# Kernel optimization log

Measured on AMD Instinct MI355X. Metric: run time of the kernel, lower is better.

## Reference

```python
import jax, jax.numpy as jnp
import numpy as np

B, IN, H = 4096, 2048, 2048
STD = 1.0 / np.sqrt(H)


def setup_inputs() -> dict:
    key = jax.random.key(0)
    ks = jax.random.split(key, 16)
    uni = lambda k, shape: jax.random.uniform(k, shape, jnp.float32, -STD, STD)
    inp = {
        "x": jax.random.normal(ks[0], (B, IN), jnp.float32),
        "h": jax.random.normal(ks[1], (B, H), jnp.float32),
        "c": jax.random.normal(ks[2], (B, H), jnp.float32),
        # weights are used untransposed via th.mm(x, w): w_x* must be [IN, H]-compatible,
        # which in the original requires IN == H; shapes kept as [H, IN].
        "w_xi": uni(ks[3], (H, IN)), "w_xf": uni(ks[4], (H, IN)),
        "w_xo": uni(ks[5], (H, IN)), "w_xc": uni(ks[6], (H, IN)),
        "w_hi": uni(ks[7], (H, H)), "w_hf": uni(ks[8], (H, H)),
        "w_ho": uni(ks[9], (H, H)), "w_hc": uni(ks[10], (H, H)),
        "b_i": uni(ks[11], (H,)), "b_f": uni(ks[12], (H,)),
        "b_o": uni(ks[13], (H,)), "b_c": uni(ks[14], (H,)),
    }
    return inp


def reference(x, h, c, w_xi, w_xf, w_xo, w_xc, w_hi, w_hf, w_ho, w_hc,
              b_i, b_f, b_o, b_c):
    # Fused form of the 8 small GEMMs: concat gate weights along output dim.
    Wx = jnp.concatenate([w_xi, w_xf, w_xo, w_xc], axis=1)  # [IN, 4H]
    Wh = jnp.concatenate([w_hi, w_hf, w_ho, w_hc], axis=1)  # [H, 4H]
    b = jnp.concatenate([b_i, b_f, b_o, b_c])               # [4H]
    gates = x @ Wx + h @ Wh + b                              # [B, 4H]
    i_t, f_t, o_t, g_t = jnp.split(gates, 4, axis=1)
    i_t = jax.nn.sigmoid(i_t)
    f_t = jax.nn.sigmoid(f_t)
    o_t = jax.nn.sigmoid(o_t)
    g_t = jnp.tanh(g_t)
    c_t = c * f_t + i_t * g_t
    h_t = o_t * jnp.tanh(c_t)
    # original reshapes to [B, 1, H]
    return h_t[:, None, :], c_t[:, None, :]
```

## Files before the change

### kernel.cpp

```cpp
#include <hip/hip_runtime.h>
#include <stdint.h>

typedef unsigned short u16;
typedef __bf16 bf16x8 __attribute__((ext_vector_type(8)));
typedef float f32x4 __attribute__((ext_vector_type(4)));
typedef unsigned short u16x8 __attribute__((ext_vector_type(8)));
typedef unsigned short u16x4 __attribute__((ext_vector_type(4)));

#define B_ROWS 4096
#define H_DIM  2048
#define K_DIM  4096
#define N_DIM  8192

__device__ __forceinline__ u16 f2b(float f) {
  union { float f; unsigned int i; } v; v.f = f;
  unsigned int i = v.i;
  return (u16)((i + 0x7fffu + ((i >> 16) & 1u)) >> 16);
}
__device__ __forceinline__ float b2f(u16 u) {
  union { unsigned int i; float f; } v; v.i = ((unsigned int)u) << 16; return v.f;
}
__device__ __forceinline__ float sigmoidf_(float x) { return 1.0f / (1.0f + __expf(-x)); }
__device__ __forceinline__ float tanhf_(float x)    { return 1.0f - 2.0f / (__expf(2.0f * x) + 1.0f); }

__device__ __forceinline__ void glds16(const u16* g, u16* l) {
  __builtin_amdgcn_global_load_lds(
      (__attribute__((address_space(1))) void*)(g),
      (__attribute__((address_space(3))) void*)(l), 16, 0, 0);
}

__device__ __forceinline__ uint32_t lds_off(const void* p) {
  return (uint32_t)(uintptr_t)(__attribute__((address_space(3))) const void*)p;
}

__device__ __forceinline__ bf16x8 ds_read128(uint32_t byte_off) {
  bf16x8 r;
  asm volatile("ds_read_b128 %0, %1" : "=&v"(r) : "v"(byte_off));
  return r;
}
#define LGKM0   asm volatile("s_waitcnt lgkmcnt(0)" ::: "memory")
#define SCHED_FENCE __builtin_amdgcn_sched_barrier(0)

struct WPtrs { const float* p[8]; };

__global__ __launch_bounds__(256) void prep_all(WPtrs wp,
                                                const float* __restrict__ X,
                                                const float* __restrict__ Hs,
                                                u16* __restrict__ Wt,
                                                u16* __restrict__ Abf) {
  __shared__ float tile[64][65];
  const int z = blockIdx.z;
  const int tid = threadIdx.x;
  if (z < 8) {
    const int s = z >> 2, g = z & 3;
    const float* __restrict__ w = wp.p[z];
    const int j0 = blockIdx.x * 64, k0 = blockIdx.y * 64;

    const int c4 = (tid & 15) * 4;
    const int r0 = tid >> 4;
#pragma unroll
    for (int it = 0; it < 4; ++it) {
      int r = r0 + it * 16;
      float4 v = *(const float4*)(w + (size_t)(k0 + r) * H_DIM + j0 + c4);
      tile[r][c4 + 0] = v.x;
      tile[r][c4 + 1] = v.y;
      tile[r][c4 + 2] = v.z;
      tile[r][c4 + 3] = v.w;
    }
    __syncthreads();

    const int cc = (tid & 7) * 8;
    const int jr0 = tid >> 3;
#pragma unroll
    for (int it = 0; it < 2; ++it) {
      int jr = jr0 + it * 32;
      u16x8 v;
#pragma unroll
      for (int i = 0; i < 8; ++i) v[i] = f2b(tile[cc + i][jr]);
      size_t orow = (size_t)(g * H_DIM + j0 + jr);
      *(u16x8*)(Wt + orow * K_DIM + (size_t)(s * H_DIM + k0 + cc)) = v;
    }
  } else {
    const int cid = (z - 8) * 1024 + blockIdx.y * 32 + blockIdx.x;
#pragma unroll
    for (int t = 0; t < 4; ++t) {
      const size_t chunk = (size_t)cid * 1024 + t * 256 + tid;
      const int b = (int)(chunk >> 9);
      const int c = ((int)chunk & 511) * 8;
      const float* src = (c < H_DIM) ? (X + (size_t)b * H_DIM + c)
                                     : (Hs + (size_t)b * H_DIM + (c - H_DIM));
      float4 v0 = *(const float4*)(src);
      float4 v1 = *(const float4*)(src + 4);
      u16x8 o;
      o[0] = f2b(v0.x); o[1] = f2b(v0.y); o[2] = f2b(v0.z); o[3] = f2b(v0.w);
      o[4] = f2b(v1.x); o[5] = f2b(v1.y); o[6] = f2b(v1.z); o[7] = f2b(v1.w);
      *(u16x8*)(Abf + chunk * 8) = o;
    }
  }
}

__global__ __launch_bounds__(512, 2) void gemm_gates(const u16* __restrict__ A,
                                                     const u16* __restrict__ Wt,
                                                     u16* __restrict__ gates) {
  __shared__ __align__(16) u16 sA[4 * 256 * 32];
  __shared__ __align__(16) u16 sB[4 * 256 * 32];
  const int tid = threadIdx.x;
  const int wave = tid >> 6, lane = tid & 63;
  const int wm = wave >> 2, wn = wave & 3;

  const int wg = (blockIdx.x & 7) * 64 + (blockIdx.x >> 3);
  const int bm = wg & 15;
  const int bn = wg >> 4;

  const int c0 = wave * 2;
  const int rs0 = c0 * 16 + (lane >> 2);
  const int rs1 = rs0 + 16;
  const int kc0 = (lane & 3) ^ ((rs0 >> 1) & 3);
  const int kc1 = (lane & 3) ^ ((rs1 >> 1) & 3);
  const size_t gA0 = (size_t)(bm * 256 + rs0) * K_DIM + kc0 * 8;
  const size_t gA1 = (size_t)(bm * 256 + rs1) * K_DIM + kc1 * 8;
  const size_t gB0 = (size_t)(bn * 256 + rs0) * K_DIM + kc0 * 8;
  const size_t gB1 = (size_t)(bn * 256 + rs1) * K_DIM + kc1 * 8;

  const int q = lane >> 4;
  uint32_t aOffB[8], bOffB[4];
#pragma unroll
  for (int i = 0; i < 8; ++i) {
    int ra = wm * 128 + i * 16 + (lane & 15);
    aOffB[i] = (uint32_t)(ra * 32 + ((q ^ ((ra >> 1) & 3)) * 8)) * 2u;
  }
#pragma unroll
  for (int i = 0; i < 4; ++i) {
    int rb = wn * 64 + i * 16 + (lane & 15);
    bOffB[i] = (uint32_t)(rb * 32 + ((q ^ ((rb >> 1) & 3)) * 8)) * 2u;
  }
  const uint32_t sAb = lds_off(sA);
  const uint32_t sBb = lds_off(sB);

  f32x4 acc[8][4] = {};
  const int NT = K_DIM / 32;

#pragma unroll
  for (int t = 0; t < 3; ++t) {
    const size_t ko = (size_t)t * 32;
    u16* da = sA + t * 8192;
    u16* db = sB + t * 8192;
    glds16(A  + gA0 + ko, da + c0 * 512);
    glds16(A  + gA1 + ko, da + (c0 + 1) * 512);
    glds16(Wt + gB0 + ko, db + c0 * 512);
    glds16(Wt + gB1 + ko, db + (c0 + 1) * 512);
  }
  asm volatile("s_waitcnt vmcnt(8)" ::: "memory");
  __builtin_amdgcn_s_barrier();

  for (int T = 0; T < NT; ++T) {
    const uint32_t aSlot = sAb + (uint32_t)(T & 3) * 16384u;
    const uint32_t bSlot = sBb + (uint32_t)(T & 3) * 16384u;
    const int pf = T + 3;
    const bool dopf = pf < NT;
    const size_t ko = (size_t)pf * 32;
    u16* dA = sA + (pf & 3) * 8192;
    u16* dB = sB + (pf & 3) * 8192;

    if (dopf) {
      glds16(A + gA0 + ko, dA + c0 * 512);
      glds16(A + gA1 + ko, dA + (c0 + 1) * 512);
    }
    bf16x8 af[4], bf[4];
#pragma unroll
    for (int i = 0; i < 4; ++i) af[i] = ds_read128(aSlot + aOffB[i]);
#pragma unroll
    for (int i = 0; i < 4; ++i) bf[i] = ds_read128(bSlot + bOffB[i]);
    __builtin_amdgcn_s_barrier();
    LGKM0;
    SCHED_FENCE;
    __builtin_amdgcn_s_setprio(1);
#pragma unroll
    for (int mi = 0; mi < 4; ++mi)
#pragma unroll
      for (int ni = 0; ni < 4; ++ni)
        acc[mi][ni] = __builtin_amdgcn_mfma_f32_16x16x32_bf16(af[mi], bf[ni], acc[mi][ni], 0, 0, 0);
    __builtin_amdgcn_s_setprio(0);

    if (dopf) {
      glds16(Wt + gB0 + ko, dB + c0 * 512);
      glds16(Wt + gB1 + ko, dB + (c0 + 1) * 512);
    }
    bf16x8 ag[4];
#pragma unroll
    for (int i = 0; i < 4; ++i) ag[i] = ds_read128(aSlot + aOffB[4 + i]);
    __builtin_amdgcn_s_barrier();
    LGKM0;
    SCHED_FENCE;
    __builtin_amdgcn_s_setprio(1);
#pragma unroll
    for (int mi = 0; mi < 4; ++mi)
#pragma unroll
      for (int ni = 0; ni < 4; ++ni)
        acc[4 + mi][ni] = __builtin_amdgcn_mfma_f32_16x16x32_bf16(ag[mi], bf[ni], acc[4 + mi][ni], 0, 0, 0);
    __builtin_amdgcn_s_setprio(0);

    if (T < NT - 3)       { asm volatile("s_waitcnt vmcnt(8)" ::: "memory"); }
    else if (T == NT - 3) { asm volatile("s_waitcnt vmcnt(4)" ::: "memory"); }
    else if (T == NT - 2) { asm volatile("s_waitcnt vmcnt(0)" ::: "memory"); }
    if (T < NT - 1) __builtin_amdgcn_s_barrier();
  }

  const int rbase = bm * 256 + wm * 128 + (lane >> 4) * 4;
  const int cbase = bn * 256 + wn * 64 + (lane & 15);
#pragma unroll
  for (int mi = 0; mi < 8; ++mi) {
#pragma unroll
    for (int ni = 0; ni < 4; ++ni) {
      size_t base = (size_t)(rbase + mi * 16) * N_DIM + (size_t)(cbase + ni * 16);
#pragma unroll
      for (int r = 0; r < 4; ++r)
        gates[base + (size_t)r * N_DIM] = f2b(acc[mi][ni][r]);
    }
  }
}

__global__ __launch_bounds__(256) void lstm_epilogue(
    const u16* __restrict__ gates, const float* __restrict__ Cin,
    const float* __restrict__ Bi, const float* __restrict__ Bf,
    const float* __restrict__ Bo, const float* __restrict__ Bc,
    float* __restrict__ Out) {
  const int idx = blockIdx.x * 256 + threadIdx.x;
  const int b = idx >> 9;
  const int j = (idx & 511) * 4;
  const size_t gbase = (size_t)b * N_DIM + j;
  u16x4 iv = *(const u16x4*)(gates + gbase);
  u16x4 fv = *(const u16x4*)(gates + gbase + 2048);
  u16x4 ov = *(const u16x4*)(gates + gbase + 4096);
  u16x4 gv = *(const u16x4*)(gates + gbase + 6144);
  float4 cv  = *(const float4*)(Cin + (size_t)b * H_DIM + j);
  float4 biv = *(const float4*)(Bi + j);
  float4 bfv = *(const float4*)(Bf + j);
  float4 bov = *(const float4*)(Bo + j);
  float4 bcv = *(const float4*)(Bc + j);
  float ce[4] = {cv.x, cv.y, cv.z, cv.w};
  float bie[4] = {biv.x, biv.y, biv.z, biv.w};
  float bfe[4] = {bfv.x, bfv.y, bfv.z, bfv.w};
  float boe[4] = {bov.x, bov.y, bov.z, bov.w};
  float bce[4] = {bcv.x, bcv.y, bcv.z, bcv.w};
  float4 hv, ctv;
  float he[4], cte[4];
#pragma unroll
  for (int e = 0; e < 4; ++e) {
    float it = sigmoidf_(b2f(iv[e]) + bie[e]);
    float ft = sigmoidf_(b2f(fv[e]) + bfe[e]);
    float ot = sigmoidf_(b2f(ov[e]) + boe[e]);
    float gt = tanhf_(b2f(gv[e]) + bce[e]);
    float ct = ce[e] * ft + it * gt;
    he[e] = ot * tanhf_(ct);
    cte[e] = ct;
  }
  hv.x = he[0]; hv.y = he[1]; hv.z = he[2]; hv.w = he[3];
  ctv.x = cte[0]; ctv.y = cte[1]; ctv.z = cte[2]; ctv.w = cte[3];
  *(float4*)(Out + (size_t)b * H_DIM + j) = hv;
  *(float4*)(Out + (size_t)B_ROWS * H_DIM + (size_t)b * H_DIM + j) = ctv;
}

extern "C" void kernel_launch(void* const* d_in, const int* in_sizes, int n_in,
                              void* d_out, int out_size, void* d_ws, size_t ws_size,
                              hipStream_t stream) {
  const float* X   = (const float*)d_in[0];
  const float* Hs  = (const float*)d_in[1];
  const float* Cin = (const float*)d_in[2];
  WPtrs wp;
  for (int i = 0; i < 8; ++i) wp.p[i] = (const float*)d_in[3 + i];
  const float* Bi = (const float*)d_in[11];
  const float* Bf = (const float*)d_in[12];
  const float* Bo = (const float*)d_in[13];
  const float* Bc = (const float*)d_in[14];

  u16* Wt    = (u16*)d_ws;
  u16* Abf   = Wt + (size_t)N_DIM * K_DIM;
  u16* gates = Abf + (size_t)B_ROWS * K_DIM;
  float* Out = (float*)d_out;

  prep_all<<<dim3(32, 32, 10), 256, 0, stream>>>(wp, X, Hs, Wt, Abf);
  gemm_gates<<<16 * 32, 512, 0, stream>>>(Abf, Wt, gates);
  lstm_epilogue<<<(B_ROWS * H_DIM / 4) / 256, 256, 0, stream>>>(gates, Cin, Bi, Bf, Bo, Bc, Out);
}
```

Baseline: 519.2 us.

## Software-pipeline LDS fragment reads across K-tiles with double-buffered B registers

Restructures the GEMM main loop so the next tile's A and B fragments are read from LDS while the second half of the current tile's MFMAs runs. B fragments ping-pong between two register sets, which needs a two-tile unrolled loop. The upper A fragments use an immediate-offset ds_read instead of separate offset registers. One barrier per tile is removed, which reduces LDS-latency stalls and synchronization, at the cost of more live registers and a more fragile waitcnt and barrier schedule.

After: 506.7 us. 2.4% less time.

```diff
diff --git a/kernel.cpp b/kernel.cpp
--- a/kernel.cpp
+++ b/kernel.cpp
@@ -38,7 +38,11 @@
   asm volatile("ds_read_b128 %0, %1" : "=&v"(r) : "v"(byte_off));
   return r;
 }
-#define LGKM0   asm volatile("s_waitcnt lgkmcnt(0)" ::: "memory")
+__device__ __forceinline__ bf16x8 ds_read128_hi(uint32_t byte_off) {
+  bf16x8 r;
+  asm volatile("ds_read_b128 %0, %1 offset:4096" : "=&v"(r) : "v"(byte_off));
+  return r;
+}
 #define SCHED_FENCE __builtin_amdgcn_sched_barrier(0)
 
 struct WPtrs { const float* p[8]; };
@@ -123,9 +127,9 @@
   const size_t gB1 = (size_t)(bn * 256 + rs1) * K_DIM + kc1 * 8;
 
   const int q = lane >> 4;
-  uint32_t aOffB[8], bOffB[4];
-#pragma unroll
-  for (int i = 0; i < 8; ++i) {
+  uint32_t aOffB[4], bOffB[4];
+#pragma unroll
+  for (int i = 0; i < 4; ++i) {
     int ra = wm * 128 + i * 16 + (lane & 15);
     aOffB[i] = (uint32_t)(ra * 32 + ((q ^ ((ra >> 1) & 3)) * 8)) * 2u;
   }
@@ -139,6 +143,8 @@
 
   f32x4 acc[8][4] = {};
   const int NT = K_DIM / 32;
+
+  bf16x8 af[4], ag[4], bfE[4], bfO[4];
 
 #pragma unroll
   for (int t = 0; t < 3; ++t) {
@@ -152,59 +158,74 @@
   }
   asm volatile("s_waitcnt vmcnt(8)" ::: "memory");
   __builtin_amdgcn_s_barrier();
-
-  for (int T = 0; T < NT; ++T) {
-    const uint32_t aSlot = sAb + (uint32_t)(T & 3) * 16384u;
-    const uint32_t bSlot = sBb + (uint32_t)(T & 3) * 16384u;
-    const int pf = T + 3;
-    const bool dopf = pf < NT;
-    const size_t ko = (size_t)pf * 32;
-    u16* dA = sA + (pf & 3) * 8192;
-    u16* dB = sB + (pf & 3) * 8192;
-
-    if (dopf) {
-      glds16(A + gA0 + ko, dA + c0 * 512);
-      glds16(A + gA1 + ko, dA + (c0 + 1) * 512);
-    }
-    bf16x8 af[4], bf[4];
-#pragma unroll
-    for (int i = 0; i < 4; ++i) af[i] = ds_read128(aSlot + aOffB[i]);
-#pragma unroll
-    for (int i = 0; i < 4; ++i) bf[i] = ds_read128(bSlot + bOffB[i]);
-    __builtin_amdgcn_s_barrier();
-    LGKM0;
-    SCHED_FENCE;
-    __builtin_amdgcn_s_setprio(1);
-#pragma unroll
-    for (int mi = 0; mi < 4; ++mi)
-#pragma unroll
-      for (int ni = 0; ni < 4; ++ni)
-        acc[mi][ni] = __builtin_amdgcn_mfma_f32_16x16x32_bf16(af[mi], bf[ni], acc[mi][ni], 0, 0, 0);
-    __builtin_amdgcn_s_setprio(0);
-
-    if (dopf) {
-      glds16(Wt + gB0 + ko, dB + c0 * 512);
-      glds16(Wt + gB1 + ko, dB + (c0 + 1) * 512);
-    }
-    bf16x8 ag[4];
-#pragma unroll
-    for (int i = 0; i < 4; ++i) ag[i] = ds_read128(aSlot + aOffB[4 + i]);
-    __builtin_amdgcn_s_barrier();
-    LGKM0;
-    SCHED_FENCE;
-    __builtin_amdgcn_s_setprio(1);
-#pragma unroll
-    for (int mi = 0; mi < 4; ++mi)
-#pragma unroll
-      for (int ni = 0; ni < 4; ++ni)
-        acc[4 + mi][ni] = __builtin_amdgcn_mfma_f32_16x16x32_bf16(ag[mi], bf[ni], acc[4 + mi][ni], 0, 0, 0);
-    __builtin_amdgcn_s_setprio(0);
-
-    if (T < NT - 3)       { asm volatile("s_waitcnt vmcnt(8)" ::: "memory"); }
-    else if (T == NT - 3) { asm volatile("s_waitcnt vmcnt(4)" ::: "memory"); }
-    else if (T == NT - 2) { asm volatile("s_waitcnt vmcnt(0)" ::: "memory"); }
-    if (T < NT - 1) __builtin_amdgcn_s_barrier();
-  }
+  SCHED_FENCE;
+#pragma unroll
+  for (int i = 0; i < 4; ++i) af[i]  = ds_read128(sAb + aOffB[i]);
+#pragma unroll
+  for (int i = 0; i < 4; ++i) bfE[i] = ds_read128(sBb + bOffB[i]);
+
+#define TILE_BODY(T, BFC, BFN)                                                 \
+  {                                                                            \
+    const int pf = (T) + 3;                                                    \
+    const uint32_t aSlot = sAb + (uint32_t)((T) & 3) * 16384u;                 \
+    const bool dopf = pf < NT;                                                 \
+    const size_t ko = (size_t)pf * 32;                                         \
+    if (dopf) {                                                                \
+      u16* dA = sA + (pf & 3) * 8192;                                          \
+      glds16(A + gA0 + ko, dA + c0 * 512);                                     \
+      glds16(A + gA1 + ko, dA + (c0 + 1) * 512);                               \
+    }                                                                          \
+                                       \
+    _Pragma("unroll")                                                          \
+    for (int i = 0; i < 4; ++i) ag[i] = ds_read128_hi(aSlot + aOffB[i]);       \
+     \
+    asm volatile("s_waitcnt lgkmcnt(4)" ::: "memory");                         \
+    SCHED_FENCE;                                                               \
+    __builtin_amdgcn_s_setprio(1);                                             \
+    _Pragma("unroll")                                                          \
+    for (int mi = 0; mi < 4; ++mi)                                             \
+      _Pragma("unroll")                                                        \
+      for (int ni = 0; ni < 4; ++ni)                                           \
+        acc[mi][ni] = __builtin_amdgcn_mfma_f32_16x16x32_bf16(                 \
+            af[mi], BFC[ni], acc[mi][ni], 0, 0, 0);                            \
+    __builtin_amdgcn_s_setprio(0);                                             \
+    if (dopf) {                                                                \
+      u16* dB = sB + (pf & 3) * 8192;                                          \
+      glds16(Wt + gB0 + ko, dB + c0 * 512);                                    \
+      glds16(Wt + gB1 + ko, dB + (c0 + 1) * 512);                              \
+    }                                                                          \
+       \
+    if ((T) < NT - 3)       { asm volatile("s_waitcnt vmcnt(8) lgkmcnt(0)" ::: "memory"); } \
+    else if ((T) == NT - 3) { asm volatile("s_waitcnt vmcnt(4) lgkmcnt(0)" ::: "memory"); } \
+    else if ((T) == NT - 2) { asm volatile("s_waitcnt vmcnt(0) lgkmcnt(0)" ::: "memory"); } \
+    else                    { asm volatile("s_waitcnt lgkmcnt(0)" ::: "memory"); }          \
+    if ((T) < NT - 1) __builtin_amdgcn_s_barrier();                            \
+    SCHED_FENCE;                                                               \
+                                  \
+    if ((T) + 1 < NT) {                                                        \
+      const uint32_t aN = sAb + (uint32_t)(((T) + 1) & 3) * 16384u;            \
+      const uint32_t bN = sBb + (uint32_t)(((T) + 1) & 3) * 16384u;            \
+      _Pragma("unroll")                                                        \
+      for (int i = 0; i < 4; ++i) af[i]  = ds_read128(aN + aOffB[i]);          \
+      _Pragma("unroll")                                                        \
+      for (int i = 0; i < 4; ++i) BFN[i] = ds_read128(bN + bOffB[i]);          \
+    }                                                                          \
+                   \
+    __builtin_amdgcn_s_setprio(1);                                             \
+    _Pragma("unroll")                                                          \
+    for (int mi = 0; mi < 4; ++mi)                                             \
+      _Pragma("unroll")                                                        \
+      for (int ni = 0; ni < 4; ++ni)                                           \
+        acc[4 + mi][ni] = __builtin_amdgcn_mfma_f32_16x16x32_bf16(             \
+            ag[mi], BFC[ni], acc[4 + mi][ni], 0, 0, 0);                        \
+    __builtin_amdgcn_s_setprio(0);                                             \
+  }
+
+  for (int T2 = 0; T2 < NT; T2 += 2) {
+    TILE_BODY(T2,     bfE, bfO);
+    TILE_BODY(T2 + 1, bfO, bfE);
+  }
+#undef TILE_BODY
 
   const int rbase = bm * 256 + wm * 128 + (lane >> 4) * 4;
   const int cbase = bn * 256 + wn * 64 + (lane & 15);
```
